# Optimization experiments

Hardware: AMD Instinct MI355X
Metric: run time of the kernel (lower is better)

## Reference

```python
import jax, jax.numpy as jnp
import numpy as np
import math

B, CIN, COUT, K, R = 8, 128, 128, 7, 2
GC = 16                     # group_channels (init arg `groups`)
G = COUT // GC              # number of dynamic-weight groups = 8
H = W = 32
EPS = 1e-5


def c4_lift(w):
    # w: [o, i, 4] -> dense 1x1 weight [o*4, i*4] via cyclic C4 shifts
    # torch: weight[:, r] = w[..., roll-by-r]  (e.g. r=1 -> [3,0,1,2])
    Wr = jnp.stack([jnp.roll(w, r, axis=-1) for r in range(4)], axis=1)  # [o,4,i,4]
    o, _, i, _ = Wr.shape
    return Wr.reshape(o * 4, i * 4)


def setup_inputs() -> dict:
    key = jax.random.key(0)
    ks = jax.random.split(key, 4)
    sc = 1.0 / math.sqrt(4 * CIN / 2)
    x = jax.random.normal(ks[0], (B, CIN * 4, H, W), dtype=jnp.float32)
    v_w = jax.random.normal(ks[1], (COUT, CIN, 4), dtype=jnp.float32) * sc
    c1_w = jax.random.normal(ks[2], (CIN // R, CIN, 4), dtype=jnp.float32) * sc
    gn_g = jnp.ones((CIN // R * 4,), jnp.float32)
    gn_b = jnp.zeros((CIN // R * 4,), jnp.float32)
    c2_w = jax.random.normal(ks[3], (K * K * G, CIN // R), dtype=jnp.float32) * (1.0 / math.sqrt(CIN // R))
    c2_b = jnp.zeros((K * K * G,), jnp.float32)
    return {"x": x, "v_w": v_w, "c1_w": c1_w, "gn_g": gn_g, "gn_b": gn_b, "c2_w": c2_w, "c2_b": c2_b}


def _forward(x, v_w, c1_w, gn_g, gn_b, c2_w, c2_b):
    b, _, h, w = x.shape
    # conv1: C4-equivariant 1x1
    t = jnp.einsum('oc,bchw->bohw', c4_lift(c1_w), x)        # [b, (CIN//R)*4, h, w]
    # GroupNorm(num_groups=CIN//R) -> normalize each group of 4 channels over (4,h,w)
    tr = t.reshape(b, CIN // R, 4, h, w)
    mu = tr.mean(axis=(2, 3, 4), keepdims=True)
    var = tr.var(axis=(2, 3, 4), keepdims=True)
    t = ((tr - mu) * jax.lax.rsqrt(var + EPS)).reshape(b, CIN // R * 4, h, w)
    t = jax.nn.relu(t * gn_g[None, :, None, None] + gn_b[None, :, None, None])
    # conv2: Conv3d 1x1 over the (c, 4) view
    tv = t.reshape(b, CIN // R, 4, h, w)
    wmap = jnp.einsum('oc,bcrhw->borhw', c2_w, tv) + c2_b[None, :, None, None, None]
    wmap = wmap.reshape(b, G, K, K, 4, h, w)
    # rotate the KxK kernel by r*90deg for C4 element r (r=0 identity)
    wmap = jnp.stack([jnp.rot90(wmap[:, :, :, :, r], k=r, axes=(2, 3)) for r in range(4)], axis=4)
    wmap = wmap.reshape(b, G, K * K, 4, h, w)                 # [b, g, p, r, h, w]
    # v branch (C4 1x1) + unfold (im2col, pad (K-1)//2, stride 1)
    v = jnp.einsum('oc,bchw->bohw', c4_lift(v_w), x)          # [b, COUT*4, h, w]
    p = (K - 1) // 2
    vp = jnp.pad(v, ((0, 0), (0, 0), (p, p), (p, p)))
    patches = jnp.stack([vp[:, :, i:i + h, j:j + w] for i in range(K) for j in range(K)], axis=2)
    patches = patches.reshape(b, G, GC, 4, K * K, h, w)       # [b, g, c, r, p, h, w]
    out = jnp.einsum('bgprhw,bgcrphw->bgcrhw', wmap, patches)
    return out.reshape(b, COUT * 4, h, w)


def reference(x, v_w, c1_w, gn_g, gn_b, c2_w, c2_b):
    return _forward(x, v_w, c1_w, gn_g, gn_b, c2_w, c2_b)
```

## Files before the change

### kernel.cpp

```cpp
#include <hip/hip_runtime.h>

#define BB   8
#define CIN  128
#define COUT 128
#define KS   7
#define HH   32
#define WWID 32
#define HW   1024
#define NG   8
#define GC   16
#define MROWS 768
#define TROWS 256
#define VROWS 512
#define KDIM 512
#define WMAP_O 392
#define WMAP_OP 448
#define C2K  64

typedef __attribute__((ext_vector_type(8))) short bf16x8;
typedef __attribute__((ext_vector_type(4))) float f32x4;

__device__ __forceinline__ short f2bf(float f) {
    unsigned u = __builtin_bit_cast(unsigned, f);
    u += 0x7fff + ((u >> 16) & 1);
    return (short)(u >> 16);
}
__device__ __forceinline__ float bf2f(unsigned short u) {
    unsigned v = (unsigned)u << 16;
    return __builtin_bit_cast(float, v);
}

__global__ __launch_bounds__(256) void prep_kernel(
    const float* __restrict__ x, const float* __restrict__ v_w,
    const float* __restrict__ c1_w, const float* __restrict__ c2_w,
    const float* __restrict__ c2_b,
    short* __restrict__ XT, short* __restrict__ Wb,
    short* __restrict__ c2wb, float* __restrict__ c2bp)
{
    __shared__ short t[64][66];
    int bx = blockIdx.x, tid = threadIdx.x;
    if (bx < 1024) {
        int b = bx >> 7, c0 = ((bx >> 4) & 7) * 64, n0 = (bx & 15) * 64;
        const float* xb = x + ((size_t)b * KDIM + c0) * HW + n0;
        #pragma unroll
        for (int l = 0; l < 16; ++l) {
            int flat = l * 256 + tid;
            int row = flat >> 6, col = flat & 63;
            t[col][row] = f2bf(xb[(size_t)row * HW + col]);
        }
        __syncthreads();
        short* xt = XT + ((size_t)b * HW + n0) * KDIM + c0;
        #pragma unroll
        for (int l = 0; l < 8; ++l) {
            int u = l * 256 + tid;
            int nrow = u >> 5, cp = (u & 31) * 2;
            short2 v = make_short2(t[nrow][cp], t[nrow][cp + 1]);
            *(short2*)(xt + (size_t)nrow * KDIM + cp) = v;
        }
    } else if (bx < 2560) {
        int idx = (bx - 1024) * 256 + tid;
        int row = idx >> 9, col = idx & 511;
        int i = col >> 2, s = col & 3;
        float val;
        if (row < 256) {
            int o = row >> 2, r = row & 3;
            val = c1_w[(o * CIN + i) * 4 + ((s - r) & 3)];
        } else {
            int ro = row - 256;
            int o = ro >> 2, r = ro & 3;
            val = v_w[(o * CIN + i) * 4 + ((s - r) & 3)];
        }
        Wb[idx] = f2bf(val);
    } else {
        int idx = (bx - 2560) * 256 + tid;
        int o = idx >> 6, k = idx & 63;
        c2wb[idx] = f2bf(o < WMAP_O ? c2_w[o * C2K + k] : 0.f);
        if (idx < WMAP_OP)
            c2bp[idx] = idx < WMAP_O ? c2_b[idx] : 0.f;
    }
}

#define GBM 64
#define GBN 128
__global__ __launch_bounds__(256) void gemm_mfma_kernel(
    const short* __restrict__ Wb, const short* __restrict__ XT,
    short* __restrict__ tvb)
{
    __shared__ short As[GBM * 32];
    __shared__ short Bs[GBN * 32];
    int b  = blockIdx.z;
    int m0 = blockIdx.y * GBM;
    int n0 = blockIdx.x * GBN;
    int tid = threadIdx.x;
    int lane = tid & 63, wv = tid >> 6;
    int wm = wv & 1, wn = wv >> 1;
    int rl = lane & 15, kg = lane >> 4;
    const short* Ab = Wb + (size_t)m0 * KDIM;
    const short* Bb = XT + ((size_t)b * HW + n0) * KDIM;
    f32x4 acc[2][4] = {};

    for (int k0 = 0; k0 < KDIM; k0 += 32) {
        {
            int c = tid;
            int row = c >> 2, kc = c & 3;
            int kcs = kc ^ ((row >> 1) & 3);
            __builtin_amdgcn_global_load_lds(
                (const __attribute__((address_space(1))) void*)(Ab + (size_t)row * KDIM + k0 + kcs * 8),
                (__attribute__((address_space(3))) void*)(As + wv * 512),
                16, 0, 0);
        }
        #pragma unroll
        for (int l = 0; l < 2; ++l) {
            int c = l * 256 + tid;
            int row = c >> 2, kc = c & 3;
            int kcs = kc ^ ((row >> 1) & 3);
            __builtin_amdgcn_global_load_lds(
                (const __attribute__((address_space(1))) void*)(Bb + (size_t)row * KDIM + k0 + kcs * 8),
                (__attribute__((address_space(3))) void*)(Bs + (l * 256 + wv * 64) * 8),
                16, 0, 0);
        }
        __syncthreads();
        bf16x8 af[2], bfr[4];
        #pragma unroll
        for (int mf = 0; mf < 2; ++mf) {
            int row = wm * 32 + mf * 16 + rl;
            af[mf] = *(const bf16x8*)(As + row * 32 + (kg ^ ((row >> 1) & 3)) * 8);
        }
        #pragma unroll
        for (int nf = 0; nf < 4; ++nf) {
            int row = wn * 64 + nf * 16 + rl;
            bfr[nf] = *(const bf16x8*)(Bs + row * 32 + (kg ^ ((row >> 1) & 3)) * 8);
        }
        #pragma unroll
        for (int mf = 0; mf < 2; ++mf)
            #pragma unroll
            for (int nf = 0; nf < 4; ++nf)
                acc[mf][nf] = __builtin_amdgcn_mfma_f32_16x16x32_bf16(af[mf], bfr[nf], acc[mf][nf], 0, 0, 0);
        __syncthreads();
    }

    short* Cb = tvb + (size_t)b * MROWS * HW;
    #pragma unroll
    for (int mf = 0; mf < 2; ++mf) {
        int rowb = m0 + wm * 32 + mf * 16 + kg * 4;
        #pragma unroll
        for (int nf = 0; nf < 4; ++nf) {
            int col = n0 + wn * 64 + nf * 16 + rl;
            #pragma unroll
            for (int i = 0; i < 4; ++i)
                Cb[(size_t)(rowb + i) * HW + col] = f2bf(acc[mf][nf][i]);
        }
    }
}

__global__ __launch_bounds__(256) void gnstats_kernel(
    const short* __restrict__ tvb, float* __restrict__ gnstat)
{
    int blk = blockIdx.x;
    int b = blk >> 6, c64 = blk & 63;
    const short* base = tvb + ((size_t)b * MROWS + c64 * 4) * HW;
    int tid = threadIdx.x;
    float s = 0.f, sq = 0.f;
    bf16x8 v0 = *(const bf16x8*)(base + tid * 16);
    bf16x8 v1 = *(const bf16x8*)(base + tid * 16 + 8);
    #pragma unroll
    for (int j = 0; j < 8; ++j) {
        float f0 = bf2f((unsigned short)v0[j]);
        float f1 = bf2f((unsigned short)v1[j]);
        s += f0 + f1; sq += f0 * f0 + f1 * f1;
    }
    __shared__ float rs[4], rq[4];
    int lane = tid & 63, wv = tid >> 6;
    #pragma unroll
    for (int off = 32; off; off >>= 1) {
        s  += __shfl_down(s, off);
        sq += __shfl_down(sq, off);
    }
    if (lane == 0) { rs[wv] = s; rq[wv] = sq; }
    __syncthreads();
    if (tid == 0) {
        float ts = rs[0] + rs[1] + rs[2] + rs[3];
        float tq = rq[0] + rq[1] + rq[2] + rq[3];
        float mu = ts * (1.f / 4096.f);
        float var = tq * (1.f / 4096.f) - mu * mu;
        gnstat[blk * 2]     = mu;
        gnstat[blk * 2 + 1] = rsqrtf(var + 1e-5f);
    }
}

__global__ __launch_bounds__(256) void tkn2_kernel(
    const short* __restrict__ tvb, const float* __restrict__ gnstat,
    const float* __restrict__ gn_g, const float* __restrict__ gn_b,
    short* __restrict__ tn)
{
    __shared__ short ts[64][72];
    __shared__ float sc[64], sh[64];
    int b4r = blockIdx.x;
    int b = b4r >> 2, r = b4r & 3;
    int hw0 = blockIdx.y * 64;
    int tid = threadIdx.x;
    if (tid < 64) {
        float mu  = gnstat[(b * 64 + tid) * 2];
        float inv = gnstat[(b * 64 + tid) * 2 + 1];
        int ch = tid * 4 + r;
        float g = gn_g[ch], bb = gn_b[ch];
        sc[tid] = inv * g;
        sh[tid] = bb - mu * inv * g;
    }
    #pragma unroll
    for (int l = 0; l < 16; ++l) {
        int flat = l * 256 + tid;
        int c = flat >> 6, hw = flat & 63;
        ts[c][hw] = tvb[((size_t)b * MROWS + c * 4 + r) * HW + hw0 + hw];
    }
    __syncthreads();
    #pragma unroll
    for (int l = 0; l < 2; ++l) {
        int u = l * 256 + tid;
        int hw = u >> 3, c0 = (u & 7) * 8;
        bf16x8 v;
        #pragma unroll
        for (int j = 0; j < 8; ++j) {
            float f = bf2f((unsigned short)ts[c0 + j][hw]);
            f = fmaxf(f * sc[c0 + j] + sh[c0 + j], 0.f);
            v[j] = f2bf(f);
        }
        *(bf16x8*)(tn + ((size_t)b4r * HW + hw0 + hw) * C2K + c0) = v;
    }
}

__global__ __launch_bounds__(256) void wmap3_kernel(
    const short* __restrict__ c2wb, const short* __restrict__ tn,
    const float* __restrict__ c2bp, short* __restrict__ wmapB)
{
    __shared__ short As[64 * 64];
    __shared__ short Bs[128 * 64];
    int n0  = blockIdx.x * 128;
    int m0  = blockIdx.y * 64;
    int b4r = blockIdx.z;
    int tid = threadIdx.x;
    int lane = tid & 63, wv = tid >> 6;
    int wm = wv & 1, wn = wv >> 1;
    int rl = lane & 15, kg = lane >> 4;
    const short* Bb = tn + ((size_t)b4r * HW + n0) * C2K;

    #pragma unroll
    for (int l = 0; l < 2; ++l) {
        int c = l * 256 + tid;
        int row = c >> 3, kc = c & 7;
        int kcs = kc ^ (row & 7);
        __builtin_amdgcn_global_load_lds(
            (const __attribute__((address_space(1))) void*)(c2wb + (size_t)(m0 + row) * C2K + kcs * 8),
            (__attribute__((address_space(3))) void*)(As + (l * 256 + wv * 64) * 8),
            16, 0, 0);
    }
    #pragma unroll
    for (int l = 0; l < 4; ++l) {
        int c = l * 256 + tid;
        int row = c >> 3, kc = c & 7;
        int kcs = kc ^ (row & 7);
        __builtin_amdgcn_global_load_lds(
            (const __attribute__((address_space(1))) void*)(Bb + (size_t)row * C2K + kcs * 8),
            (__attribute__((address_space(3))) void*)(Bs + (l * 256 + wv * 64) * 8),
            16, 0, 0);
    }
    __syncthreads();

    f32x4 acc[2][4] = {};
    #pragma unroll
    for (int ks = 0; ks < 2; ++ks) {
        bf16x8 af[2], bfr[4];
        #pragma unroll
        for (int mf = 0; mf < 2; ++mf) {
            int row = wm * 32 + mf * 16 + rl;
            af[mf] = *(const bf16x8*)(As + row * 64 + ((ks * 4 + kg) ^ (row & 7)) * 8);
        }
        #pragma unroll
        for (int nf = 0; nf < 4; ++nf) {
            int row = wn * 64 + nf * 16 + rl;
            bfr[nf] = *(const bf16x8*)(Bs + row * 64 + ((ks * 4 + kg) ^ (row & 7)) * 8);
        }
        #pragma unroll
        for (int mf = 0; mf < 2; ++mf)
            #pragma unroll
            for (int nf = 0; nf < 4; ++nf)
                acc[mf][nf] = __builtin_amdgcn_mfma_f32_16x16x32_bf16(af[mf], bfr[nf], acc[mf][nf], 0, 0, 0);
    }

    short* wb = wmapB + (size_t)b4r * WMAP_OP * HW;
    #pragma unroll
    for (int mf = 0; mf < 2; ++mf) {
        int rowb = m0 + wm * 32 + mf * 16 + kg * 4;
        float bi[4];
        #pragma unroll
        for (int i = 0; i < 4; ++i) bi[i] = c2bp[rowb + i];
        #pragma unroll
        for (int nf = 0; nf < 4; ++nf) {
            int col = n0 + wn * 64 + nf * 16 + rl;
            #pragma unroll
            for (int i = 0; i < 4; ++i)
                wb[(size_t)(rowb + i) * HW + col] = f2bf(acc[mf][nf][i] + bi[i]);
        }
    }
}

__global__ __launch_bounds__(256, 4) void agg4_kernel(
    const short* __restrict__ tvb, const short* __restrict__ wmapB,
    float* __restrict__ out)
{
    __shared__ float vt[8][15][44];
    int bx = blockIdx.x;
    int b = bx >> 5;
    int g = (bx >> 2) & 7;
    int r = bx & 3;
    int h0   = blockIdx.y * 8;
    int half = blockIdx.z;
    int tid  = threadIdx.x;
    int w0q = tid & 7, hb = (tid >> 3) & 1, cc4 = (tid >> 4) & 3, cq = tid >> 6;
    int hl = cq * 2 + hb;
    int h = h0 + hl, w0 = w0q * 4;

    int A, Bc, Cc;
    if      (r == 0) { A = 0;  Bc = 7;  Cc = 1;  }
    else if (r == 1) { A = 6;  Bc = -1; Cc = 7;  }
    else if (r == 2) { A = 48; Bc = -7; Cc = -1; }
    else             { A = 42; Bc = 1;  Cc = -7; }

    const short* vpb = tvb + ((size_t)b * MROWS + TROWS) * HW;
    for (int idx = tid; idx < 8 * 15 * 44; idx += 256) {
        int cc  = idx / 660;
        int rem = idx - cc * 660;
        int row = rem / 44, col = rem - row * 44;
        int gh = h0 - 3 + row, gw = col - 4;
        int ch = (g * GC + half * 8 + cc) * 4 + r;
        float v = 0.f;
        if (gh >= 0 && gh < HH && gw >= 0 && gw < WWID)
            v = bf2f((unsigned short)vpb[(size_t)ch * HW + gh * WWID + gw]);
        vt[cc][row][col] = v;
    }
    __syncthreads();

    const short* wmb = wmapB + ((size_t)(b * 4 + r) * WMAP_OP + g * 49) * HW + h * WWID + w0;
    float acc[2][4] = {};
    #pragma unroll
    for (int di = 0; di < 7; ++di) {
        float wrf[7][4];
        #pragma unroll
        for (int dj = 0; dj < 7; ++dj) {
            int porig = A + Bc * di + Cc * dj;
            ushort4 wv = *(const ushort4*)(wmb + (size_t)porig * HW);
            wrf[dj][0] = bf2f(wv.x); wrf[dj][1] = bf2f(wv.y);
            wrf[dj][2] = bf2f(wv.z); wrf[dj][3] = bf2f(wv.w);
        }
        #pragma unroll
        for (int c2 = 0; c2 < 2; ++c2) {
            int hc = cc4 * 2 + c2;
            const float* rp = &vt[hc][hl + di][w0];
            float4 q0 = *(const float4*)(rp);
            float4 q1 = *(const float4*)(rp + 4);
            float4 q2 = *(const float4*)(rp + 8);
            float win[12] = {q0.x, q0.y, q0.z, q0.w,
                             q1.x, q1.y, q1.z, q1.w,
                             q2.x, q2.y, q2.z, q2.w};
            #pragma unroll
            for (int dj = 0; dj < 7; ++dj)
                #pragma unroll
                for (int px = 0; px < 4; ++px)
                    acc[c2][px] += wrf[dj][px] * win[px + dj + 1];
        }
    }
    #pragma unroll
    for (int c2 = 0; c2 < 2; ++c2) {
        int ch = (g * GC + half * 8 + cc4 * 2 + c2) * 4 + r;
        float4 o4 = make_float4(acc[c2][0], acc[c2][1], acc[c2][2], acc[c2][3]);
        *(float4*)(out + ((size_t)b * 512 + ch) * HW + h * WWID + w0) = o4;
    }
}

extern "C" void kernel_launch(void* const* d_in, const int* in_sizes, int n_in,
                              void* d_out, int out_size, void* d_ws, size_t ws_size,
                              hipStream_t stream)
{
    const float* x    = (const float*)d_in[0];
    const float* v_w  = (const float*)d_in[1];
    const float* c1_w = (const float*)d_in[2];
    const float* gn_g = (const float*)d_in[3];
    const float* gn_b = (const float*)d_in[4];
    const float* c2_w = (const float*)d_in[5];
    const float* c2_b = (const float*)d_in[6];
    float* out = (float*)d_out;

    char* p = (char*)d_ws;
    short* Wb     = (short*)p;           p += (size_t)MROWS * KDIM * 2;
    short* tvb    = (short*)p;           p += (size_t)BB * MROWS * HW * 2;
    short* wmapB  = (short*)p;           p += (size_t)32 * WMAP_OP * HW * 2;
    short* XT     = (short*)wmapB;
    short* tn     = (short*)p;           p += (size_t)32 * HW * C2K * 2;
    short* c2wb   = (short*)p;           p += (size_t)WMAP_OP * C2K * 2;
    float* c2bp   = (float*)p;           p += (size_t)WMAP_OP * 4;
    float* gnstat = (float*)p;           p += (size_t)512 * 2 * 4;

    prep_kernel     <<<2672, 256, 0, stream>>>(x, v_w, c1_w, c2_w, c2_b, XT, Wb, c2wb, c2bp);
    gemm_mfma_kernel<<<dim3(HW / GBN, MROWS / GBM, BB), 256, 0, stream>>>(Wb, XT, tvb);
    gnstats_kernel  <<<512, 256, 0, stream>>>(tvb, gnstat);
    tkn2_kernel     <<<dim3(32, 16), 256, 0, stream>>>(tvb, gnstat, gn_g, gn_b, tn);
    wmap3_kernel    <<<dim3(HW / 128, WMAP_OP / 64, 32), 256, 0, stream>>>(c2wb, tn, c2bp, wmapB);
    agg4_kernel     <<<dim3(BB * NG * 4, 4, 2), 256, 0, stream>>>(tvb, wmapB, out);
}
```

Baseline: 76.35 us.

## Fuse GroupNorm stats into GEMM, widen K tile, merge agg halves

The standalone gnstats kernel is removed: the GEMM epilogue reduces per-group sums and sums of squares from fp32 accumulators and atomically adds them into a buffer that prep zeroes, and tkn2 derives mean and inverse std. The GEMM K tile grows from 32 to 64 with a wider XOR swizzle, halving barrier count per K. The aggregation kernel now handles all 16 channels per block instead of splitting into two halves, with vectorized halo loads, reusing each wmap load across twice as many channels at the cost of more LDS and registers (launch bounds lowered to 3). Atomics make the stats order-dependent in floating point.

```diff
diff --git a/kernel.cpp b/kernel.cpp
--- a/kernel.cpp
+++ b/kernel.cpp
@@ -35,7 +35,8 @@
     const float* __restrict__ c1_w, const float* __restrict__ c2_w,
     const float* __restrict__ c2_b,
     short* __restrict__ XT, short* __restrict__ Wb,
-    short* __restrict__ c2wb, float* __restrict__ c2bp)
+    short* __restrict__ c2wb, float* __restrict__ c2bp,
+    float* __restrict__ gnstat)
 {
     __shared__ short t[64][66];
     int bx = blockIdx.x, tid = threadIdx.x;
@@ -71,23 +72,26 @@
             val = v_w[(o * CIN + i) * 4 + ((s - r) & 3)];
         }
         Wb[idx] = f2bf(val);
-    } else {
+    } else if (bx < 2672) {
         int idx = (bx - 2560) * 256 + tid;
         int o = idx >> 6, k = idx & 63;
         c2wb[idx] = f2bf(o < WMAP_O ? c2_w[o * C2K + k] : 0.f);
         if (idx < WMAP_OP)
             c2bp[idx] = idx < WMAP_O ? c2_b[idx] : 0.f;
+    } else {
+        *(float4*)(gnstat + tid * 4) = make_float4(0.f, 0.f, 0.f, 0.f);
     }
 }
 
 #define GBM 64
 #define GBN 128
+#define GBK 64
 __global__ __launch_bounds__(256) void gemm_mfma_kernel(
     const short* __restrict__ Wb, const short* __restrict__ XT,
-    short* __restrict__ tvb)
-{
-    __shared__ short As[GBM * 32];
-    __shared__ short Bs[GBN * 32];
+    short* __restrict__ tvb, float* __restrict__ gnstat)
+{
+    __shared__ short As[GBM * GBK];
+    __shared__ short Bs[GBN * GBK];
     int b  = blockIdx.z;
     int m0 = blockIdx.y * GBM;
     int n0 = blockIdx.x * GBN;
@@ -99,43 +103,47 @@
     const short* Bb = XT + ((size_t)b * HW + n0) * KDIM;
     f32x4 acc[2][4] = {};
 
-    for (int k0 = 0; k0 < KDIM; k0 += 32) {
-        {
-            int c = tid;
-            int row = c >> 2, kc = c & 3;
-            int kcs = kc ^ ((row >> 1) & 3);
+    for (int k0 = 0; k0 < KDIM; k0 += GBK) {
+        #pragma unroll
+        for (int l = 0; l < 2; ++l) {
+            int c = l * 256 + tid;
+            int row = c >> 3, kc = c & 7;
+            int kcs = kc ^ (row & 7);
             __builtin_amdgcn_global_load_lds(
                 (const __attribute__((address_space(1))) void*)(Ab + (size_t)row * KDIM + k0 + kcs * 8),
-                (__attribute__((address_space(3))) void*)(As + wv * 512),
+                (__attribute__((address_space(3))) void*)(As + (l * 256 + wv * 64) * 8),
                 16, 0, 0);
         }
         #pragma unroll
-        for (int l = 0; l < 2; ++l) {
+        for (int l = 0; l < 4; ++l) {
             int c = l * 256 + tid;
-            int row = c >> 2, kc = c & 3;
-            int kcs = kc ^ ((row >> 1) & 3);
+            int row = c >> 3, kc = c & 7;
+            int kcs = kc ^ (row & 7);
             __builtin_amdgcn_global_load_lds(
                 (const __attribute__((address_space(1))) void*)(Bb + (size_t)row * KDIM + k0 + kcs * 8),
                 (__attribute__((address_space(3))) void*)(Bs + (l * 256 + wv * 64) * 8),
                 16, 0, 0);
         }
         __syncthreads();
-        bf16x8 af[2], bfr[4];
-        #pragma unroll
-        for (int mf = 0; mf < 2; ++mf) {
-            int row = wm * 32 + mf * 16 + rl;
-            af[mf] = *(const bf16x8*)(As + row * 32 + (kg ^ ((row >> 1) & 3)) * 8);
-        }
-        #pragma unroll
-        for (int nf = 0; nf < 4; ++nf) {
-            int row = wn * 64 + nf * 16 + rl;
-            bfr[nf] = *(const bf16x8*)(Bs + row * 32 + (kg ^ ((row >> 1) & 3)) * 8);
-        }
-        #pragma unroll
-        for (int mf = 0; mf < 2; ++mf)
-            #pragma unroll
-            for (int nf = 0; nf < 4; ++nf)
-                acc[mf][nf] = __builtin_amdgcn_mfma_f32_16x16x32_bf16(af[mf], bfr[nf], acc[mf][nf], 0, 0, 0);
+        #pragma unroll
+        for (int ks = 0; ks < 2; ++ks) {
+            bf16x8 af[2], bfr[4];
+            #pragma unroll
+            for (int mf = 0; mf < 2; ++mf) {
+                int row = wm * 32 + mf * 16 + rl;
+                af[mf] = *(const bf16x8*)(As + row * GBK + ((ks * 4 + kg) ^ (row & 7)) * 8);
+            }
+            #pragma unroll
+            for (int nf = 0; nf < 4; ++nf) {
+                int row = wn * 64 + nf * 16 + rl;
+                bfr[nf] = *(const bf16x8*)(Bs + row * GBK + ((ks * 4 + kg) ^ (row & 7)) * 8);
+            }
+            #pragma unroll
+            for (int mf = 0; mf < 2; ++mf)
+                #pragma unroll
+                for (int nf = 0; nf < 4; ++nf)
+                    acc[mf][nf] = __builtin_amdgcn_mfma_f32_16x16x32_bf16(af[mf], bfr[nf], acc[mf][nf], 0, 0, 0);
+        }
         __syncthreads();
     }
 
@@ -151,40 +159,29 @@
                 Cb[(size_t)(rowb + i) * HW + col] = f2bf(acc[mf][nf][i]);
         }
     }
-}
-
-__global__ __launch_bounds__(256) void gnstats_kernel(
-    const short* __restrict__ tvb, float* __restrict__ gnstat)
-{
-    int blk = blockIdx.x;
-    int b = blk >> 6, c64 = blk & 63;
-    const short* base = tvb + ((size_t)b * MROWS + c64 * 4) * HW;
-    int tid = threadIdx.x;
-    float s = 0.f, sq = 0.f;
-    bf16x8 v0 = *(const bf16x8*)(base + tid * 16);
-    bf16x8 v1 = *(const bf16x8*)(base + tid * 16 + 8);
-    #pragma unroll
-    for (int j = 0; j < 8; ++j) {
-        float f0 = bf2f((unsigned short)v0[j]);
-        float f1 = bf2f((unsigned short)v1[j]);
-        s += f0 + f1; sq += f0 * f0 + f1 * f1;
-    }
-    __shared__ float rs[4], rq[4];
-    int lane = tid & 63, wv = tid >> 6;
-    #pragma unroll
-    for (int off = 32; off; off >>= 1) {
-        s  += __shfl_down(s, off);
-        sq += __shfl_down(sq, off);
-    }
-    if (lane == 0) { rs[wv] = s; rq[wv] = sq; }
-    __syncthreads();
-    if (tid == 0) {
-        float ts = rs[0] + rs[1] + rs[2] + rs[3];
-        float tq = rq[0] + rq[1] + rq[2] + rq[3];
-        float mu = ts * (1.f / 4096.f);
-        float var = tq * (1.f / 4096.f) - mu * mu;
-        gnstat[blk * 2]     = mu;
-        gnstat[blk * 2 + 1] = rsqrtf(var + 1e-5f);
+
+    if (m0 < TROWS) {
+        #pragma unroll
+        for (int mf = 0; mf < 2; ++mf) {
+            float s = 0.f, sq = 0.f;
+            #pragma unroll
+            for (int nf = 0; nf < 4; ++nf)
+                #pragma unroll
+                for (int i = 0; i < 4; ++i) {
+                    float v = acc[mf][nf][i];
+                    s += v; sq += v * v;
+                }
+            #pragma unroll
+            for (int m = 1; m <= 8; m <<= 1) {
+                s  += __shfl_xor(s, m);
+                sq += __shfl_xor(sq, m);
+            }
+            if (rl == 0) {
+                int grp = (m0 + wm * 32 + mf * 16 + kg * 4) >> 2;
+                atomicAdd(&gnstat[(b * 64 + grp) * 2],     s);
+                atomicAdd(&gnstat[(b * 64 + grp) * 2 + 1], sq);
+            }
+        }
     }
 }
 
@@ -200,8 +197,11 @@
     int hw0 = blockIdx.y * 64;
     int tid = threadIdx.x;
     if (tid < 64) {
-        float mu  = gnstat[(b * 64 + tid) * 2];
-        float inv = gnstat[(b * 64 + tid) * 2 + 1];
+        float s   = gnstat[(b * 64 + tid) * 2];
+        float sq  = gnstat[(b * 64 + tid) * 2 + 1];
+        float mu  = s * (1.f / 4096.f);
+        float var = sq * (1.f / 4096.f) - mu * mu;
+        float inv = rsqrtf(var + 1e-5f);
         int ch = tid * 4 + r;
         float g = gn_g[ch], bb = gn_b[ch];
         sc[tid] = inv * g;
@@ -304,18 +304,17 @@
     }
 }
 
-__global__ __launch_bounds__(256, 4) void agg4_kernel(
+__global__ __launch_bounds__(256, 3) void agg5_kernel(
     const short* __restrict__ tvb, const short* __restrict__ wmapB,
     float* __restrict__ out)
 {
-    __shared__ float vt[8][15][44];
+    __shared__ float vt[16][15][44];
     int bx = blockIdx.x;
     int b = bx >> 5;
     int g = (bx >> 2) & 7;
     int r = bx & 3;
-    int h0   = blockIdx.y * 8;
-    int half = blockIdx.z;
-    int tid  = threadIdx.x;
+    int h0  = blockIdx.y * 8;
+    int tid = threadIdx.x;
     int w0q = tid & 7, hb = (tid >> 3) & 1, cc4 = (tid >> 4) & 3, cq = tid >> 6;
     int hl = cq * 2 + hb;
     int h = h0 + hl, w0 = w0q * 4;
@@ -327,21 +326,30 @@
     else             { A = 42; Bc = 1;  Cc = -7; }
 
     const short* vpb = tvb + ((size_t)b * MROWS + TROWS) * HW;
-    for (int idx = tid; idx < 8 * 15 * 44; idx += 256) {
-        int cc  = idx / 660;
-        int rem = idx - cc * 660;
-        int row = rem / 44, col = rem - row * 44;
-        int gh = h0 - 3 + row, gw = col - 4;
-        int ch = (g * GC + half * 8 + cc) * 4 + r;
-        float v = 0.f;
-        if (gh >= 0 && gh < HH && gw >= 0 && gw < WWID)
-            v = bf2f((unsigned short)vpb[(size_t)ch * HW + gh * WWID + gw]);
-        vt[cc][row][col] = v;
+    for (int e = tid; e < 16 * 15 * 3; e += 256) {
+        int cc  = e / 45;
+        int rem = e - cc * 45;
+        int row = rem / 3, q = rem - row * 3;
+        int col = (q == 0) ? 0 : (36 + (q - 1) * 4);
+        *(float4*)(&vt[cc][row][col]) = make_float4(0.f, 0.f, 0.f, 0.f);
+    }
+    for (int f = tid; f < 16 * 15 * 8; f += 256) {
+        int cc  = f / 120;
+        int rem = f - cc * 120;
+        int row = rem >> 3, q = rem & 7;
+        int gh = h0 - 3 + row;
+        float4 v4 = make_float4(0.f, 0.f, 0.f, 0.f);
+        if (gh >= 0 && gh < HH) {
+            int ch = (g * GC + cc) * 4 + r;
+            ushort4 u = *(const ushort4*)(vpb + (size_t)ch * HW + gh * WWID + q * 4);
+            v4 = make_float4(bf2f(u.x), bf2f(u.y), bf2f(u.z), bf2f(u.w));
+        }
+        *(float4*)(&vt[cc][row][4 + q * 4]) = v4;
     }
     __syncthreads();
 
     const short* wmb = wmapB + ((size_t)(b * 4 + r) * WMAP_OP + g * 49) * HW + h * WWID + w0;
-    float acc[2][4] = {};
+    float acc[4][4] = {};
     #pragma unroll
     for (int di = 0; di < 7; ++di) {
         float wrf[7][4];
@@ -353,8 +361,8 @@
             wrf[dj][2] = bf2f(wv.z); wrf[dj][3] = bf2f(wv.w);
         }
         #pragma unroll
-        for (int c2 = 0; c2 < 2; ++c2) {
-            int hc = cc4 * 2 + c2;
+        for (int c2 = 0; c2 < 4; ++c2) {
+            int hc = cc4 * 4 + c2;
             const float* rp = &vt[hc][hl + di][w0];
             float4 q0 = *(const float4*)(rp);
             float4 q1 = *(const float4*)(rp + 4);
@@ -370,8 +378,8 @@
         }
     }
     #pragma unroll
-    for (int c2 = 0; c2 < 2; ++c2) {
-        int ch = (g * GC + half * 8 + cc4 * 2 + c2) * 4 + r;
+    for (int c2 = 0; c2 < 4; ++c2) {
+        int ch = (g * GC + cc4 * 4 + c2) * 4 + r;
         float4 o4 = make_float4(acc[c2][0], acc[c2][1], acc[c2][2], acc[c2][3]);
         *(float4*)(out + ((size_t)b * 512 + ch) * HW + h * WWID + w0) = o4;
     }
@@ -400,10 +408,9 @@
     float* c2bp   = (float*)p;           p += (size_t)WMAP_OP * 4;
     float* gnstat = (float*)p;           p += (size_t)512 * 2 * 4;
 
-    prep_kernel     <<<2672, 256, 0, stream>>>(x, v_w, c1_w, c2_w, c2_b, XT, Wb, c2wb, c2bp);
-    gemm_mfma_kernel<<<dim3(HW / GBN, MROWS / GBM, BB), 256, 0, stream>>>(Wb, XT, tvb);
-    gnstats_kernel  <<<512, 256, 0, stream>>>(tvb, gnstat);
+    prep_kernel     <<<2673, 256, 0, stream>>>(x, v_w, c1_w, c2_w, c2_b, XT, Wb, c2wb, c2bp, gnstat);
+    gemm_mfma_kernel<<<dim3(HW / GBN, MROWS / GBM, BB), 256, 0, stream>>>(Wb, XT, tvb, gnstat);
     tkn2_kernel     <<<dim3(32, 16), 256, 0, stream>>>(tvb, gnstat, gn_g, gn_b, tn);
     wmap3_kernel    <<<dim3(HW / 128, WMAP_OP / 64, 32), 256, 0, stream>>>(c2wb, tn, c2bp, wmapB);
-    agg4_kernel     <<<dim3(BB * NG * 4, 4, 2), 256, 0, stream>>>(tvb, wmapB, out);
-}
+    agg5_kernel     <<<dim3(BB * NG * 4, 4), 256, 0, stream>>>(tvb, wmapB, out);
+}
```

Result: faster. 63.17 us (-17.3%).
